# Performance work log

Measured on AMD Instinct MI355X. Metric: run time of the kernel, lower is better.

## Reference

```python
import jax, jax.numpy as jnp
import numpy as np

# ---- static config (seq_lens / is_prefill are Python lists in the original) ----
HIDDEN, H, D = 4096, 32, 128
SEQ = 1024            # prefill length / decode history length
N_PRE, N_DEC = 4, 4
T = N_PRE * SEQ + N_DEC            # 4100 total tokens
SEQ_LENS = [SEQ] * N_PRE + [SEQ] * N_DEC
IS_PREFILL = [True] * N_PRE + [False] * N_DEC
NUM_SLOTS = 8192
MAX_LEN, ROPE_BASE = 8192, 10000.0
SCALE = D ** -0.5


def _rope_tables():
    inv_freq = 1.0 / (ROPE_BASE ** (np.arange(0, D, 2, dtype=np.float32) / D))
    t = np.arange(MAX_LEN, dtype=np.float32)
    freqs = np.outer(t, inv_freq)
    emb = np.concatenate([freqs, freqs], axis=-1)  # [MAX_LEN, D]
    return jnp.asarray(np.cos(emb), jnp.float32), jnp.asarray(np.sin(emb), jnp.float32)

COS_T, SIN_T = _rope_tables()


def rotate_half(x):
    x1, x2 = jnp.split(x, 2, axis=-1)
    return jnp.concatenate([-x2, x1], axis=-1)


def setup_inputs() -> dict:
    key = jax.random.key(0)
    k1, k2, k3 = jax.random.split(key, 3)
    x = jax.random.normal(k1, (T, HIDDEN), jnp.float32)
    # positions: prefill seqs get 0..SEQ-1, decode seqs are at position SEQ
    pos = np.concatenate([np.tile(np.arange(SEQ), N_PRE), np.full(N_DEC, SEQ)]).astype(np.int64)
    positions = jnp.asarray(pos)
    slot_mapping = jnp.arange(T, dtype=jnp.int64)
    k_cache = jnp.zeros((NUM_SLOTS, H, D), jnp.float32)
    v_cache = jnp.zeros((NUM_SLOTS, H, D), jnp.float32)
    w_qkv = jax.random.normal(k2, (HIDDEN, 3 * H * D), jnp.float32) * 0.02
    w_out = jax.random.normal(k3, (H * D, HIDDEN), jnp.float32) * 0.02
    return {"x": x, "k_cache": k_cache, "v_cache": v_cache, "w_qkv": w_qkv,
            "w_out": w_out, "positions": positions, "slot_mapping": slot_mapping}


def reference(x, k_cache, v_cache, w_qkv, w_out, positions, slot_mapping):
    qkv = x @ w_qkv                                   # [T, 3*H*D]
    q, k, v = jnp.split(qkv, 3, axis=-1)
    q = q.reshape(T, H, D)
    k = k.reshape(T, H, D)
    v = v.reshape(T, H, D)
    cos = COS_T[positions][:, None, :]                # [T, 1, D]
    sin = SIN_T[positions][:, None, :]
    q = q * cos + rotate_half(q) * sin
    k = k * cos + rotate_half(k) * sin
    # scatter new k/v into flat paged cache
    kc = k_cache.at[slot_mapping].set(k)
    vc = v_cache.at[slot_mapping].set(v)

    outs = []
    off = 0
    for seq_len, prefill in zip(SEQ_LENS, IS_PREFILL):
        nq = seq_len if prefill else 1
        q_i = q[off:off + nq]                         # [nq, H, D]
        if prefill:
            k_i, v_i = k[off:off + nq], v[off:off + nq]
            attn = jnp.einsum('qhd,khd->hqk', q_i, k_i) * SCALE
            mask = jnp.triu(jnp.full((nq, nq), -jnp.inf, jnp.float32), 1)
            attn = jax.nn.softmax(attn + mask, axis=-1)
            out = jnp.einsum('hqk,khd->qhd', attn, v_i).reshape(nq, H * D)
        else:
            k_h, v_h = kc[:seq_len], vc[:seq_len]     # history from cache
            attn = jnp.einsum('qhd,khd->hqk', q_i, k_h) * SCALE
            attn = jax.nn.softmax(attn, axis=-1)
            out = jnp.einsum('hqk,khd->qhd', attn, v_h).reshape(1, H * D)
        outs.append(out)
        off += nq
    return jnp.concatenate(outs, axis=0) @ w_out      # [T, HIDDEN]
```

## Files before the change

kernel.cpp:

```cpp
#include <hip/hip_runtime.h>

#define T_TOK 4100
#define MMAIN 4096
#define HID   4096
#define NH    32
#define DH    128
#define NQKV  12288
#define ATT_SCALE 0.08838834764831845f
#define NEG_BIG  (-3.0e38f)

typedef unsigned short ushort_t;
typedef __attribute__((ext_vector_type(8))) short bf16x8;
typedef __attribute__((ext_vector_type(4))) float f32x4;

typedef const void __attribute__((address_space(1)))* gas_ptr;
typedef void __attribute__((address_space(3)))* las_ptr;

__device__ __forceinline__ ushort_t f2bf(float f){
  unsigned int u = __builtin_bit_cast(unsigned int, f);
  u = u + 0x7FFFu + ((u >> 16) & 1u);
  return (ushort_t)(u >> 16);
}
__device__ __forceinline__ float bf2f(ushort_t h){
  unsigned int u = ((unsigned int)h) << 16;
  return __builtin_bit_cast(float, u);
}
__device__ __forceinline__ f32x4 mfma16(bf16x8 a, bf16x8 b, f32x4 c){
  return __builtin_amdgcn_mfma_f32_16x16x32_bf16(a, b, c, 0, 0, 0);
}
__device__ __forceinline__ void gload_lds16(const void* g, void* l){
  __builtin_amdgcn_global_load_lds((gas_ptr)g, (las_ptr)l, 16, 0, 0);
}


__global__ void convert_x(const float* __restrict__ x, ushort_t* __restrict__ xb){
  const long i4 = (long)blockIdx.x * 256 + threadIdx.x;
  if (i4 >= (long)T_TOK * HID / 4) return;
  const long i = i4 * 4;
  const float4 v = *(const float4*)(x + i);
  union { ushort_t u[4]; uint2 w; } o;
  o.u[0] = f2bf(v.x); o.u[1] = f2bf(v.y); o.u[2] = f2bf(v.z); o.u[3] = f2bf(v.w);
  *(uint2*)(xb + i) = o.w;
}

__global__ void tconv(const float* __restrict__ W, ushort_t* __restrict__ WT, int R, int C){
  __shared__ float tile[32][33];
  const int bc = blockIdx.x, br = blockIdx.y;
  const int tid = threadIdx.x;
  const int cl = tid & 31, rl = tid >> 5;
  const long c = (long)bc * 32 + cl;
#pragma unroll
  for (int j = 0; j < 32; j += 8)
    tile[rl + j][cl] = W[((long)br * 32 + rl + j) * C + c];
  __syncthreads();
#pragma unroll
  for (int j = 0; j < 32; j += 8)
    WT[((long)bc * 32 + rl + j) * R + (long)br * 32 + cl] = f2bf(tile[cl][rl + j]);
}


#define MFMAQ(QM,QN,BARR)                                                         \
  _Pragma("unroll")                                                               \
  for (int mi = 0; mi < 4; ++mi) {                                                \
    _Pragma("unroll")                                                             \
    for (int ni = 0; ni < 2; ++ni) {                                              \
      acc[QM][QN][mi][ni] = mfma16(af[mi][0], BARR[ni][0], acc[QM][QN][mi][ni]);  \
      acc[QM][QN][mi][ni] = mfma16(af[mi][1], BARR[ni][1], acc[QM][QN][mi][ni]);  \
    } }

template<bool OUT_BF16>
__global__ void __launch_bounds__(512, 2)
gemm256(const ushort_t* __restrict__ A, const ushort_t* __restrict__ B,
        ushort_t* __restrict__ Cb, float* __restrict__ Cf,
        int N, int K, int GM, int Mvalid)
{
  extern __shared__ char smem[];
  char* smA = smem;
  char* smB = smem + 65536;

  const int nwg = gridDim.x;
  int bid = blockIdx.x;
  bid = (bid & 7) * (nwg >> 3) + (bid >> 3);
  const int bm = bid % GM, bn = bid / GM;

  const int tid = threadIdx.x;
  const int wid = tid >> 6, lane = tid & 63;
  const int wm = wid >> 2, wn = wid & 3;
  const int l16 = lane & 15, g = lane >> 4;
  const int lr = lane >> 3, lu = lane & 7;

  const long arow0 = (long)bm * 256;
  const long brow0 = (long)bn * 256;

  const ushort_t* aS[4]; const ushort_t* bS[4];
#pragma unroll
  for (int cc = 0; cc < 4; ++cc){
    aS[cc] = A + (arow0 + cc*64 + wid*8 + lr) * (long)K + (lu ^ lr) * 8;
    bS[cc] = B + (brow0 + cc*64 + wid*8 + lr) * (long)K + (lu ^ lr) * 8;
  }

  auto stageA = [&](int buf, int cc, long kt){
    gload_lds16(aS[cc] + kt, smA + buf*32768 + (cc*64 + wid*8)*128);
  };
  auto stageB = [&](int buf, int cc, long kt){
    gload_lds16(bS[cc] + kt, smB + buf*32768 + (cc*64 + wid*8)*128);
  };
  auto ldA = [&](int buf, int qm, int mi, int ks) -> bf16x8 {
    const int row = qm*128 + wm*64 + mi*16 + l16;
    return *(const bf16x8*)(smA + buf*32768 + row*128 + (((ks*4+g) ^ (l16&7))*16));
  };
  auto ldB = [&](int buf, int qn, int ni, int ks) -> bf16x8 {
    const int row = qn*128 + wn*32 + ni*16 + l16;
    return *(const bf16x8*)(smB + buf*32768 + row*128 + (((ks*4+g) ^ (l16&7))*16));
  };

  f32x4 acc[2][2][4][2];
#pragma unroll
  for (int a_ = 0; a_ < 2; ++a_)
#pragma unroll
  for (int b_ = 0; b_ < 2; ++b_)
#pragma unroll
  for (int c_ = 0; c_ < 4; ++c_)
#pragma unroll
  for (int d_ = 0; d_ < 2; ++d_) acc[a_][b_][c_][d_] = (f32x4){0.f,0.f,0.f,0.f};

  bf16x8 af[4][2], bf0[2][2], bf1[2][2];
  const int NT = K >> 6;

  stageA(0,0,0); stageA(0,1,0);
  stageB(0,0,0); stageB(0,1,0);
  stageB(0,2,0); stageB(0,3,0);
  stageA(0,2,0); stageA(0,3,0);
  asm volatile("s_waitcnt vmcnt(4)" ::: "memory");
  __builtin_amdgcn_s_barrier();

  auto tile = [&](int buf, long ktn){
    asm volatile("s_waitcnt vmcnt(2)" ::: "memory");
#pragma unroll
    for (int mi = 0; mi < 4; ++mi){ af[mi][0] = ldA(buf,0,mi,0); af[mi][1] = ldA(buf,0,mi,1); }
#pragma unroll
    for (int ni = 0; ni < 2; ++ni){ bf0[ni][0] = ldB(buf,0,ni,0); bf0[ni][1] = ldB(buf,0,ni,1); }
    stageA(buf^1, 0, ktn); stageA(buf^1, 1, ktn);
    __builtin_amdgcn_s_barrier();
    asm volatile("s_waitcnt lgkmcnt(0)" ::: "memory");
    __builtin_amdgcn_sched_barrier(0);
    __builtin_amdgcn_s_setprio(1);
    MFMAQ(0,0,bf0);
    __builtin_amdgcn_s_setprio(0);
    asm volatile("s_waitcnt vmcnt(2)" ::: "memory");
#pragma unroll
    for (int ni = 0; ni < 2; ++ni){ bf1[ni][0] = ldB(buf,1,ni,0); bf1[ni][1] = ldB(buf,1,ni,1); }
    stageB(buf^1, 0, ktn); stageB(buf^1, 1, ktn);
    __builtin_amdgcn_s_barrier();
    asm volatile("s_waitcnt lgkmcnt(0)" ::: "memory");
    __builtin_amdgcn_sched_barrier(0);
    __builtin_amdgcn_s_setprio(1);
    MFMAQ(0,1,bf1);
    __builtin_amdgcn_s_setprio(0);
#pragma unroll
    for (int mi = 0; mi < 4; ++mi){ af[mi][0] = ldA(buf,1,mi,0); af[mi][1] = ldA(buf,1,mi,1); }
    stageB(buf^1, 2, ktn); stageB(buf^1, 3, ktn);
    __builtin_amdgcn_s_barrier();
    asm volatile("s_waitcnt lgkmcnt(0)" ::: "memory");
    __builtin_amdgcn_sched_barrier(0);
    __builtin_amdgcn_s_setprio(1);
    MFMAQ(1,1,bf1);
    __builtin_amdgcn_s_setprio(0);
    asm volatile("s_waitcnt vmcnt(2)" ::: "memory");
    stageA(buf^1, 2, ktn); stageA(buf^1, 3, ktn);
    __builtin_amdgcn_s_barrier();
    __builtin_amdgcn_sched_barrier(0);
    __builtin_amdgcn_s_setprio(1);
    MFMAQ(1,0,bf0);
    __builtin_amdgcn_s_setprio(0);
  };

  for (int t = 0; t < NT; t += 2){
    const long k1 = (long)(t+1) * 64;
    const long k2 = (long)((t+2 < NT) ? (t+2) : (NT-1)) * 64;
    tile(0, k1);
    tile(1, k2);
  }
  asm volatile("s_waitcnt vmcnt(0)" ::: "memory");

#pragma unroll
  for (int qm = 0; qm < 2; ++qm)
#pragma unroll
  for (int qn = 0; qn < 2; ++qn)
#pragma unroll
  for (int mi = 0; mi < 4; ++mi)
#pragma unroll
  for (int ni = 0; ni < 2; ++ni)
#pragma unroll
  for (int r = 0; r < 4; ++r){
    const long row = arow0 + qm*128 + wm*64 + mi*16 + g*4 + r;
    const long col = brow0 + qn*128 + wn*32 + ni*16 + l16;
    if (OUT_BF16){
      Cb[row * N + col] = f2bf(acc[qm][qn][mi][ni][r]);
    } else {
      if (row < Mvalid) Cf[row * N + col] = acc[qm][qn][mi][ni][r];
    }
  }
}


__global__ void __launch_bounds__(256, 8)
gemv_tail(const ushort_t* __restrict__ A, const ushort_t* __restrict__ B,
          ushort_t* __restrict__ Cb, float* __restrict__ Cf, int ldc)
{
  const int col  = blockIdx.x * 4 + (threadIdx.x >> 6);
  const int lane = threadIdx.x & 63;
  const ushort_t* brow  = B + (long)col * HID + lane * 64;
  const ushort_t* abase = A + 4096L * HID + lane * 64;
  float acc0 = 0.f, acc1 = 0.f, acc2 = 0.f, acc3 = 0.f;
#pragma unroll
  for (int i = 0; i < 8; ++i){
    union { bf16x8 v; short s[8]; } bv, a0, a1, a2, a3;
    bv.v = *(const bf16x8*)(brow + i*8);
    a0.v = *(const bf16x8*)(abase + 0L*HID + i*8);
    a1.v = *(const bf16x8*)(abase + 1L*HID + i*8);
    a2.v = *(const bf16x8*)(abase + 2L*HID + i*8);
    a3.v = *(const bf16x8*)(abase + 3L*HID + i*8);
#pragma unroll
    for (int e = 0; e < 8; ++e){
      const float bf_ = bf2f((ushort_t)bv.s[e]);
      acc0 += bf2f((ushort_t)a0.s[e]) * bf_;
      acc1 += bf2f((ushort_t)a1.s[e]) * bf_;
      acc2 += bf2f((ushort_t)a2.s[e]) * bf_;
      acc3 += bf2f((ushort_t)a3.s[e]) * bf_;
    }
  }
#pragma unroll
  for (int off = 32; off; off >>= 1){
    acc0 += __shfl_xor(acc0, off);
    acc1 += __shfl_xor(acc1, off);
    acc2 += __shfl_xor(acc2, off);
    acc3 += __shfl_xor(acc3, off);
  }
  if (lane == 0){
    if (Cb){
      Cb[4096L*ldc + col] = f2bf(acc0);
      Cb[4097L*ldc + col] = f2bf(acc1);
      Cb[4098L*ldc + col] = f2bf(acc2);
      Cb[4099L*ldc + col] = f2bf(acc3);
    } else {
      Cf[4096L*ldc + col] = acc0;
      Cf[4097L*ldc + col] = acc1;
      Cf[4098L*ldc + col] = acc2;
      Cf[4099L*ldc + col] = acc3;
    }
  }
}


__global__ void rope_scatter(ushort_t* __restrict__ qkv,
                             const int* __restrict__ pos32,
                             const int* __restrict__ slot32,
                             ushort_t* __restrict__ kcw, ushort_t* __restrict__ vcw)
{
  const long gi = (long)blockIdx.x * 256 + threadIdx.x;
  if (gi >= (long)T_TOK * NH * 64) return;
  const int  i = gi & 63;
  const int  h = (gi >> 6) & 31;
  const long t = gi >> 11;

  const bool p64 = (pos32[1] == 0);
  const bool s64 = (slot32[1] == 0);
  const long pv   = p64 ? ((const long long*)pos32)[t]  : (long)pos32[t];
  const long slot = s64 ? ((const long long*)slot32)[t] : (long)slot32[t];

  const float inv = exp2f(-(float)i * 0.2076187116f);
  const float ang = (float)pv * inv;
  float sn, cs;
  __sincosf(ang, &sn, &cs);

  ushort_t* base = qkv + t * (long)NQKV + h * DH + i;
  const float q1 = bf2f(base[0]), q2 = bf2f(base[64]);
  base[0]  = f2bf(q1 * cs - q2 * sn);
  base[64] = f2bf(q2 * cs + q1 * sn);

  ushort_t* kb = base + HID;
  const float k1 = bf2f(kb[0]), k2 = bf2f(kb[64]);
  const float k1n = k1 * cs - k2 * sn, k2n = k2 * cs + k1 * sn;
  kb[0]  = f2bf(k1n);
  kb[64] = f2bf(k2n);

  if (slot >= 0 && slot < 1024){
    ushort_t* kd = kcw + (slot * NH + h) * DH + i;
    kd[0] = f2bf(k1n); kd[64] = f2bf(k2n);
    const ushort_t* vsrc = base + 2 * HID;
    ushort_t* vd = vcw + (slot * NH + h) * DH + i;
    vd[0] = vsrc[0]; vd[64] = vsrc[64];
  }
}


__global__ void __launch_bounds__(256, 3)
attn_prefill(const ushort_t* __restrict__ qkv, ushort_t* __restrict__ attn)
{
  __shared__ ushort_t Ks[64][128];
  __shared__ ushort_t Vt[128][72];
  __shared__ ushort_t Ps[4][16][72];
  const int qb = blockIdx.x, h = blockIdx.y, sq = blockIdx.z;
  const long tok0 = (long)sq * 1024;
  const int tid = threadIdx.x, wid = tid >> 6, lane = tid & 63;
  const int l16 = lane & 15, g = lane >> 4;
  const int q0 = qb * 64;

  bf16x8 qf[4];
  {
    const ushort_t* qrow = qkv + (tok0 + q0 + wid*16 + l16) * (long)NQKV + h * DH;
#pragma unroll
    for (int dc = 0; dc < 4; ++dc) qf[dc] = *(const bf16x8*)(qrow + dc*32 + g*8);
  }

  f32x4 oacc[8];
#pragma unroll
  for (int i = 0; i < 8; i++) oacc[i] = (f32x4){0.f, 0.f, 0.f, 0.f};
  float mrow[4] = {NEG_BIG, NEG_BIG, NEG_BIG, NEG_BIG};
  float lrow[4] = {0.f, 0.f, 0.f, 0.f};

  const int nkb = qb + 1;
  for (int kb = 0; kb < nkb; ++kb){
    __syncthreads();
    {
      const ushort_t* kbase = qkv + (tok0 + kb*64) * (long)NQKV + HID + h * DH;
#pragma unroll
      for (int c = 0; c < 4; ++c){
        const int row = c*16 + wid*4 + g;
        const int pu = (l16 & 8) | ((l16 ^ (row & 7)) & 7);
        gload_lds16(kbase + (long)row * NQKV + pu*8, &Ks[c*16 + wid*4][0]);
      }
    }
    {
      const int key4 = (tid & 15) * 4;
      const int dg8  = tid >> 4;
      const ushort_t* vbase = qkv + (tok0 + kb*64) * (long)NQKV + 2*HID + h*DH + dg8*8;
      union { bf16x8 v; short s[8]; } vr[4];
#pragma unroll
      for (int j = 0; j < 4; ++j)
        vr[j].v = *(const bf16x8*)(vbase + (long)(key4 + j) * NQKV);
#pragma unroll
      for (int e = 0; e < 8; ++e){
        union { ushort_t u[4]; uint2 w; } o;
        o.u[0] = (ushort_t)vr[0].s[e]; o.u[1] = (ushort_t)vr[1].s[e];
        o.u[2] = (ushort_t)vr[2].s[e]; o.u[3] = (ushort_t)vr[3].s[e];
        *(uint2*)&Vt[dg8*8 + e][key4] = o.w;
      }
    }
    __syncthreads();

    if (kb*64 <= q0 + wid*16 + 15){
      f32x4 sfr[4];
#pragma unroll
      for (int nf = 0; nf < 4; ++nf) sfr[nf] = (f32x4){0.f,0.f,0.f,0.f};
#pragma unroll
      for (int nf = 0; nf < 4; ++nf){
#pragma unroll
        for (int dc = 0; dc < 4; ++dc){
          const int uu = dc*4 + g;
          const int pu = (uu & 8) | ((uu ^ (l16 & 7)) & 7);
          bf16x8 kf = *(const bf16x8*)&Ks[nf*16 + l16][pu * 8];
          sfr[nf] = mfma16(qf[dc], kf, sfr[nf]);
        }
      }
      float alpha[4];
#pragma unroll
      for (int r = 0; r < 4; r++){
        const int qg = q0 + wid*16 + g*4 + r;
        float s[4];
#pragma unroll
        for (int nf = 0; nf < 4; ++nf){
          s[nf] = sfr[nf][r] * ATT_SCALE;
          if (kb*64 + nf*16 + l16 > qg) s[nf] = NEG_BIG;
        }
        float mx = fmaxf(fmaxf(s[0], s[1]), fmaxf(s[2], s[3]));
        mx = fmaxf(mx, __shfl_xor(mx, 1));
        mx = fmaxf(mx, __shfl_xor(mx, 2));
        mx = fmaxf(mx, __shfl_xor(mx, 4));
        mx = fmaxf(mx, __shfl_xor(mx, 8));
        const float mn = fmaxf(mrow[r], mx);
        const float al = __expf(mrow[r] - mn);
        float p[4], rs = 0.f;
#pragma unroll
        for (int nf = 0; nf < 4; ++nf){ p[nf] = __expf(s[nf] - mn); rs += p[nf]; }
        rs += __shfl_xor(rs, 1);
        rs += __shfl_xor(rs, 2);
        rs += __shfl_xor(rs, 4);
        rs += __shfl_xor(rs, 8);
        lrow[r] = lrow[r] * al + rs;
        mrow[r] = mn;
        alpha[r] = al;
#pragma unroll
        for (int nf = 0; nf < 4; ++nf)
          Ps[wid][g*4 + r][nf*16 + l16] = f2bf(p[nf]);
      }
#pragma unroll
      for (int df = 0; df < 8; ++df){
        f32x4 o = oacc[df];
        o[0] *= alpha[0]; o[1] *= alpha[1]; o[2] *= alpha[2]; o[3] *= alpha[3];
        oacc[df] = o;
      }
#pragma unroll
      for (int ks = 0; ks < 2; ++ks){
        bf16x8 pa = *(const bf16x8*)&Ps[wid][l16][ks*32 + g*8];
#pragma unroll
        for (int df = 0; df < 8; ++df){
          bf16x8 vf = *(const bf16x8*)&Vt[df*16 + l16][ks*32 + g*8];
          oacc[df] = mfma16(pa, vf, oacc[df]);
        }
      }
    }
  }

#pragma unroll
  for (int df = 0; df < 8; ++df){
#pragma unroll
    for (int r = 0; r < 4; ++r){
      const long row = tok0 + q0 + wid*16 + g*4 + r;
      attn[row * HID + h*DH + df*16 + l16] = f2bf(oacc[df][r] / lrow[r]);
    }
  }
}


__global__ void __launch_bounds__(256, 2)
attn_decode(const ushort_t* __restrict__ qkv, const ushort_t* __restrict__ kcw,
            const ushort_t* __restrict__ vcw, ushort_t* __restrict__ attn)
{
  const int h = blockIdx.x;
  const long t = 4096 + blockIdx.y;
  __shared__ float qs[128];
  __shared__ float ps[1024];
  __shared__ float red[8];
  __shared__ float oh[128];
  const int tid = threadIdx.x, wid = tid >> 6, lane = tid & 63;
  if (tid < 128) qs[tid] = bf2f(qkv[t * (long)NQKV + h*DH + tid]);
  __syncthreads();
  float sv[4];
#pragma unroll
  for (int j = 0; j < 4; j++){
    const int key = tid + j*256;
    const ushort_t* kr = kcw + ((long)key * NH + h) * DH;
    float acc = 0.f;
    for (int d = 0; d < 128; d += 8){
      union { bf16x8 v; short s[8]; } uu;
      uu.v = *(const bf16x8*)(kr + d);
#pragma unroll
      for (int e = 0; e < 8; e++) acc += qs[d+e] * bf2f((ushort_t)uu.s[e]);
    }
    sv[j] = acc * ATT_SCALE;
  }
  float mx = fmaxf(fmaxf(sv[0], sv[1]), fmaxf(sv[2], sv[3]));
#pragma unroll
  for (int off = 1; off < 64; off <<= 1) mx = fmaxf(mx, __shfl_xor(mx, off));
  if (lane == 0) red[wid] = mx;
  __syncthreads();
  const float gmax = fmaxf(fmaxf(red[0], red[1]), fmaxf(red[2], red[3]));
  float psum = 0.f;
#pragma unroll
  for (int j = 0; j < 4; j++){
    const float p = __expf(sv[j] - gmax);
    ps[tid + j*256] = p;
    psum += p;
  }
#pragma unroll
  for (int off = 1; off < 64; off <<= 1) psum += __shfl_xor(psum, off);
  if (lane == 0) red[4 + wid] = psum;
  __syncthreads();
  const float gsum = red[4] + red[5] + red[6] + red[7];
  const int d = tid & 127, half = tid >> 7;
  float acc = 0.f;
  for (int key = half*512; key < half*512 + 512; ++key)
    acc += ps[key] * bf2f(vcw[((long)key * NH + h) * DH + d]);
  if (half) oh[d] = acc;
  __syncthreads();
  if (!half) attn[t * HID + h*DH + d] = f2bf((acc + oh[d]) / gsum);
}


extern "C" void kernel_launch(void* const* d_in, const int* in_sizes, int n_in,
                              void* d_out, int out_size, void* d_ws, size_t ws_size,
                              hipStream_t stream) {
  const float* x      = (const float*)d_in[0];
  const float* wqkv   = (const float*)d_in[3];
  const float* wout   = (const float*)d_in[4];
  const int*   pos    = (const int*)d_in[5];
  const int*   slots  = (const int*)d_in[6];

  char* ws = (char*)d_ws;
  ushort_t* xb    = (ushort_t*)(ws);
  ushort_t* qkvb  = (ushort_t*)(ws + 35651584L);
  ushort_t* wqkvT = (ushort_t*)(ws + 142606336L);
  ushort_t* attnb = (ushort_t*)(ws + 142606336L);
  ushort_t* woutT = (ushort_t*)(ws + 243269632L);
  ushort_t* kcw   = (ushort_t*)(ws + 276824064L);
  ushort_t* vcw   = (ushort_t*)(ws + 285212672L);

  hipFuncSetAttribute((const void*)gemm256<true>,
                      hipFuncAttributeMaxDynamicSharedMemorySize, 131072);
  hipFuncSetAttribute((const void*)gemm256<false>,
                      hipFuncAttributeMaxDynamicSharedMemorySize, 131072);

  convert_x<<<16400, 256, 0, stream>>>(x, xb);
  tconv<<<dim3(NQKV/32, HID/32), 256, 0, stream>>>(wqkv, wqkvT, HID, NQKV);
  tconv<<<dim3(HID/32, HID/32), 256, 0, stream>>>(wout, woutT, HID, HID);

  gemm256<true><<<(MMAIN/256)*(NQKV/256), 512, 131072, stream>>>(
      xb, wqkvT, qkvb, nullptr, NQKV, HID, MMAIN/256, MMAIN);
  gemv_tail<<<NQKV/4, 256, 0, stream>>>(xb, wqkvT, qkvb, nullptr, NQKV);

  rope_scatter<<<32800, 256, 0, stream>>>(qkvb, pos, slots, kcw, vcw);

  attn_prefill<<<dim3(16, NH, 4), 256, 0, stream>>>(qkvb, attnb);
  attn_decode<<<dim3(NH, 4), 256, 0, stream>>>(qkvb, kcw, vcw, attnb);

  gemm256<false><<<(MMAIN/256)*(HID/256), 512, 131072, stream>>>(
      attnb, woutT, nullptr, (float*)d_out, HID, HID, MMAIN/256, MMAIN);
  gemv_tail<<<HID/4, 256, 0, stream>>>(attnb, woutT, nullptr, (float*)d_out, HID);

  (void)in_sizes; (void)n_in; (void)out_size; (void)ws_size;
}
```

Before: 1.004 ms.

## Fold GEMV tails into GEMM grids and fuse decode into prefill attention

```diff
diff --git a/kernel.cpp b/kernel.cpp
--- a/kernel.cpp
+++ b/kernel.cpp
@@ -78,13 +78,63 @@
   char* smA = smem;
   char* smB = smem + 65536;
 
-  const int nwg = gridDim.x;
-  int bid = blockIdx.x;
-  bid = (bid & 7) * (nwg >> 3) + (bid >> 3);
-  const int bm = bid % GM, bn = bid / GM;
-
   const int tid = threadIdx.x;
   const int wid = tid >> 6, lane = tid & 63;
+  const int ngemm = GM * (N >> 8);
+
+  if ((int)blockIdx.x >= ngemm){
+    const int tb = blockIdx.x - ngemm;
+    const int colbase = (tb*8 + wid) * 16;
+    const ushort_t* arow = A + 4096L * K + lane * 64;
+    for (int cc = 0; cc < 16; ++cc){
+      const int col = colbase + cc;
+      const ushort_t* brow = B + (long)col * K + lane * 64;
+      float a0=0.f, a1=0.f, a2=0.f, a3=0.f;
+#pragma unroll
+      for (int i = 0; i < 8; ++i){
+        union { bf16x8 v; short s[8]; } bv, r0, r1, r2, r3;
+        bv.v = *(const bf16x8*)(brow + i*8);
+        r0.v = *(const bf16x8*)(arow + 0L*K + i*8);
+        r1.v = *(const bf16x8*)(arow + 1L*K + i*8);
+        r2.v = *(const bf16x8*)(arow + 2L*K + i*8);
+        r3.v = *(const bf16x8*)(arow + 3L*K + i*8);
+#pragma unroll
+        for (int e = 0; e < 8; ++e){
+          const float bf_ = bf2f((ushort_t)bv.s[e]);
+          a0 += bf2f((ushort_t)r0.s[e]) * bf_;
+          a1 += bf2f((ushort_t)r1.s[e]) * bf_;
+          a2 += bf2f((ushort_t)r2.s[e]) * bf_;
+          a3 += bf2f((ushort_t)r3.s[e]) * bf_;
+        }
+      }
+#pragma unroll
+      for (int off = 32; off; off >>= 1){
+        a0 += __shfl_xor(a0, off);
+        a1 += __shfl_xor(a1, off);
+        a2 += __shfl_xor(a2, off);
+        a3 += __shfl_xor(a3, off);
+      }
+      if (lane == 0){
+        if (OUT_BF16){
+          Cb[4096L*N + col] = f2bf(a0);
+          Cb[4097L*N + col] = f2bf(a1);
+          Cb[4098L*N + col] = f2bf(a2);
+          Cb[4099L*N + col] = f2bf(a3);
+        } else {
+          Cf[4096L*N + col] = a0;
+          Cf[4097L*N + col] = a1;
+          Cf[4098L*N + col] = a2;
+          Cf[4099L*N + col] = a3;
+        }
+      }
+    }
+    return;
+  }
+
+  int bid = blockIdx.x;
+  bid = (bid & 7) * (ngemm >> 3) + (bid >> 3);
+  const int bm = bid % GM, bn = bid / GM;
+
   const int wm = wid >> 2, wn = wid & 3;
   const int l16 = lane & 15, g = lane >> 4;
   const int lr = lane >> 3, lu = lane & 7;
@@ -204,55 +254,6 @@
 }
 
 
-__global__ void __launch_bounds__(256, 8)
-gemv_tail(const ushort_t* __restrict__ A, const ushort_t* __restrict__ B,
-          ushort_t* __restrict__ Cb, float* __restrict__ Cf, int ldc)
-{
-  const int col  = blockIdx.x * 4 + (threadIdx.x >> 6);
-  const int lane = threadIdx.x & 63;
-  const ushort_t* brow  = B + (long)col * HID + lane * 64;
-  const ushort_t* abase = A + 4096L * HID + lane * 64;
-  float acc0 = 0.f, acc1 = 0.f, acc2 = 0.f, acc3 = 0.f;
-#pragma unroll
-  for (int i = 0; i < 8; ++i){
-    union { bf16x8 v; short s[8]; } bv, a0, a1, a2, a3;
-    bv.v = *(const bf16x8*)(brow + i*8);
-    a0.v = *(const bf16x8*)(abase + 0L*HID + i*8);
-    a1.v = *(const bf16x8*)(abase + 1L*HID + i*8);
-    a2.v = *(const bf16x8*)(abase + 2L*HID + i*8);
-    a3.v = *(const bf16x8*)(abase + 3L*HID + i*8);
-#pragma unroll
-    for (int e = 0; e < 8; ++e){
-      const float bf_ = bf2f((ushort_t)bv.s[e]);
-      acc0 += bf2f((ushort_t)a0.s[e]) * bf_;
-      acc1 += bf2f((ushort_t)a1.s[e]) * bf_;
-      acc2 += bf2f((ushort_t)a2.s[e]) * bf_;
-      acc3 += bf2f((ushort_t)a3.s[e]) * bf_;
-    }
-  }
-#pragma unroll
-  for (int off = 32; off; off >>= 1){
-    acc0 += __shfl_xor(acc0, off);
-    acc1 += __shfl_xor(acc1, off);
-    acc2 += __shfl_xor(acc2, off);
-    acc3 += __shfl_xor(acc3, off);
-  }
-  if (lane == 0){
-    if (Cb){
-      Cb[4096L*ldc + col] = f2bf(acc0);
-      Cb[4097L*ldc + col] = f2bf(acc1);
-      Cb[4098L*ldc + col] = f2bf(acc2);
-      Cb[4099L*ldc + col] = f2bf(acc3);
-    } else {
-      Cf[4096L*ldc + col] = acc0;
-      Cf[4097L*ldc + col] = acc1;
-      Cf[4098L*ldc + col] = acc2;
-      Cf[4099L*ldc + col] = acc3;
-    }
-  }
-}
-
-
 __global__ void rope_scatter(ushort_t* __restrict__ qkv,
                              const int* __restrict__ pos32,
                              const int* __restrict__ slot32,
@@ -296,14 +297,67 @@
 
 
 __global__ void __launch_bounds__(256, 3)
-attn_prefill(const ushort_t* __restrict__ qkv, ushort_t* __restrict__ attn)
+attn_fused(const ushort_t* __restrict__ qkv, const ushort_t* __restrict__ kcw,
+           const ushort_t* __restrict__ vcw, ushort_t* __restrict__ attn)
 {
-  __shared__ ushort_t Ks[64][128];
-  __shared__ ushort_t Vt[128][72];
-  __shared__ ushort_t Ps[4][16][72];
+  __shared__ char sm[44032];
   const int qb = blockIdx.x, h = blockIdx.y, sq = blockIdx.z;
+  const int tid = threadIdx.x, wid = tid >> 6, lane = tid & 63;
+
+  if (qb == 16){
+    float* qs  = (float*)sm;
+    float* ps  = qs + 128;
+    float* red = ps + 1024;
+    float* oh  = red + 8;
+    const long t = 4096 + sq;
+    if (tid < 128) qs[tid] = bf2f(qkv[t * (long)NQKV + h*DH + tid]);
+    __syncthreads();
+    float sv[4];
+#pragma unroll
+    for (int j = 0; j < 4; j++){
+      const int key = tid + j*256;
+      const ushort_t* kr = kcw + ((long)key * NH + h) * DH;
+      float acc = 0.f;
+      for (int d = 0; d < 128; d += 8){
+        union { bf16x8 v; short s[8]; } uu;
+        uu.v = *(const bf16x8*)(kr + d);
+#pragma unroll
+        for (int e = 0; e < 8; e++) acc += qs[d+e] * bf2f((ushort_t)uu.s[e]);
+      }
+      sv[j] = acc * ATT_SCALE;
+    }
+    float mx = fmaxf(fmaxf(sv[0], sv[1]), fmaxf(sv[2], sv[3]));
+#pragma unroll
+    for (int off = 1; off < 64; off <<= 1) mx = fmaxf(mx, __shfl_xor(mx, off));
+    if (lane == 0) red[wid] = mx;
+    __syncthreads();
+    const float gmax = fmaxf(fmaxf(red[0], red[1]), fmaxf(red[2], red[3]));
+    float psum = 0.f;
+#pragma unroll
+    for (int j = 0; j < 4; j++){
+      const float p = __expf(sv[j] - gmax);
+      ps[tid + j*256] = p;
+      psum += p;
+    }
+#pragma unroll
+    for (int off = 1; off < 64; off <<= 1) psum += __shfl_xor(psum, off);
+    if (lane == 0) red[4 + wid] = psum;
+    __syncthreads();
+    const float gsum = red[4] + red[5] + red[6] + red[7];
+    const int d = tid & 127, half = tid >> 7;
+    float acc = 0.f;
+    for (int key = half*512; key < half*512 + 512; ++key)
+      acc += ps[key] * bf2f(vcw[((long)key * NH + h) * DH + d]);
+    if (half) oh[d] = acc;
+    __syncthreads();
+    if (!half) attn[t * HID + h*DH + d] = f2bf((acc + oh[d]) / gsum);
+    return;
+  }
+
+  ushort_t (*Ks)[128]    = (ushort_t(*)[128])sm;
+  ushort_t (*Vt)[72]     = (ushort_t(*)[72])(sm + 16384);
+  ushort_t (*Ps)[16][72] = (ushort_t(*)[16][72])(sm + 34816);
   const long tok0 = (long)sq * 1024;
-  const int tid = threadIdx.x, wid = tid >> 6, lane = tid & 63;
   const int l16 = lane & 15, g = lane >> 4;
   const int q0 = qb * 64;
 
@@ -350,7 +404,7 @@
     }
     __syncthreads();
 
-    if (kb*64 <= q0 + wid*16 + 15){
+    {
       f32x4 sfr[4];
 #pragma unroll
       for (int nf = 0; nf < 4; ++nf) sfr[nf] = (f32x4){0.f,0.f,0.f,0.f};
@@ -364,15 +418,18 @@
           sfr[nf] = mfma16(qf[dc], kf, sfr[nf]);
         }
       }
+      const bool diag = (kb == qb);
       float alpha[4];
 #pragma unroll
       for (int r = 0; r < 4; r++){
-        const int qg = q0 + wid*16 + g*4 + r;
         float s[4];
 #pragma unroll
-        for (int nf = 0; nf < 4; ++nf){
-          s[nf] = sfr[nf][r] * ATT_SCALE;
-          if (kb*64 + nf*16 + l16 > qg) s[nf] = NEG_BIG;
+        for (int nf = 0; nf < 4; ++nf) s[nf] = sfr[nf][r] * ATT_SCALE;
+        if (diag){
+          const int qg = q0 + wid*16 + g*4 + r;
+#pragma unroll
+          for (int nf = 0; nf < 4; ++nf)
+            if (kb*64 + nf*16 + l16 > qg) s[nf] = NEG_BIG;
         }
         float mx = fmaxf(fmaxf(s[0], s[1]), fmaxf(s[2], s[3]));
         mx = fmaxf(mx, __shfl_xor(mx, 1));
@@ -424,61 +481,6 @@
 }
 
 
-__global__ void __launch_bounds__(256, 2)
-attn_decode(const ushort_t* __restrict__ qkv, const ushort_t* __restrict__ kcw,
-            const ushort_t* __restrict__ vcw, ushort_t* __restrict__ attn)
-{
-  const int h = blockIdx.x;
-  const long t = 4096 + blockIdx.y;
-  __shared__ float qs[128];
-  __shared__ float ps[1024];
-  __shared__ float red[8];
-  __shared__ float oh[128];
-  const int tid = threadIdx.x, wid = tid >> 6, lane = tid & 63;
-  if (tid < 128) qs[tid] = bf2f(qkv[t * (long)NQKV + h*DH + tid]);
-  __syncthreads();
-  float sv[4];
-#pragma unroll
-  for (int j = 0; j < 4; j++){
-    const int key = tid + j*256;
-    const ushort_t* kr = kcw + ((long)key * NH + h) * DH;
-    float acc = 0.f;
-    for (int d = 0; d < 128; d += 8){
-      union { bf16x8 v; short s[8]; } uu;
-      uu.v = *(const bf16x8*)(kr + d);
-#pragma unroll
-      for (int e = 0; e < 8; e++) acc += qs[d+e] * bf2f((ushort_t)uu.s[e]);
-    }
-    sv[j] = acc * ATT_SCALE;
-  }
-  float mx = fmaxf(fmaxf(sv[0], sv[1]), fmaxf(sv[2], sv[3]));
-#pragma unroll
-  for (int off = 1; off < 64; off <<= 1) mx = fmaxf(mx, __shfl_xor(mx, off));
-  if (lane == 0) red[wid] = mx;
-  __syncthreads();
-  const float gmax = fmaxf(fmaxf(red[0], red[1]), fmaxf(red[2], red[3]));
-  float psum = 0.f;
-#pragma unroll
-  for (int j = 0; j < 4; j++){
-    const float p = __expf(sv[j] - gmax);
-    ps[tid + j*256] = p;
-    psum += p;
-  }
-#pragma unroll
-  for (int off = 1; off < 64; off <<= 1) psum += __shfl_xor(psum, off);
-  if (lane == 0) red[4 + wid] = psum;
-  __syncthreads();
-  const float gsum = red[4] + red[5] + red[6] + red[7];
-  const int d = tid & 127, half = tid >> 7;
-  float acc = 0.f;
-  for (int key = half*512; key < half*512 + 512; ++key)
-    acc += ps[key] * bf2f(vcw[((long)key * NH + h) * DH + d]);
-  if (half) oh[d] = acc;
-  __syncthreads();
-  if (!half) attn[t * HID + h*DH + d] = f2bf((acc + oh[d]) / gsum);
-}
-
-
 extern "C" void kernel_launch(void* const* d_in, const int* in_sizes, int n_in,
                               void* d_out, int out_size, void* d_ws, size_t ws_size,
                               hipStream_t stream) {
@@ -506,18 +508,15 @@
   tconv<<<dim3(NQKV/32, HID/32), 256, 0, stream>>>(wqkv, wqkvT, HID, NQKV);
   tconv<<<dim3(HID/32, HID/32), 256, 0, stream>>>(wout, woutT, HID, HID);
 
-  gemm256<true><<<(MMAIN/256)*(NQKV/256), 512, 131072, stream>>>(
+  gemm256<true><<<(MMAIN/256)*(NQKV/256) + NQKV/128, 512, 131072, stream>>>(
       xb, wqkvT, qkvb, nullptr, NQKV, HID, MMAIN/256, MMAIN);
-  gemv_tail<<<NQKV/4, 256, 0, stream>>>(xb, wqkvT, qkvb, nullptr, NQKV);
 
   rope_scatter<<<32800, 256, 0, stream>>>(qkvb, pos, slots, kcw, vcw);
 
-  attn_prefill<<<dim3(16, NH, 4), 256, 0, stream>>>(qkvb, attnb);
-  attn_decode<<<dim3(NH, 4), 256, 0, stream>>>(qkvb, kcw, vcw, attnb);
-
-  gemm256<false><<<(MMAIN/256)*(HID/256), 512, 131072, stream>>>(
+  attn_fused<<<dim3(17, NH, 4), 256, 0, stream>>>(qkvb, kcw, vcw, attnb);
+
+  gemm256<false><<<(MMAIN/256)*(HID/256) + HID/128, 512, 131072, stream>>>(
       attnb, woutT, nullptr, (float*)d_out, HID, HID, MMAIN/256, MMAIN);
-  gemv_tail<<<HID/4, 256, 0, stream>>>(attnb, woutT, nullptr, (float*)d_out, HID);
 
   (void)in_sizes; (void)n_in; (void)out_size; (void)ws_size;
 }
```

Measured after the change: 964.7 us. -3.9%, faster.

## Fuse decode attention into prefill kernel and skip unused decode K/V work

Applied to the files above, without the earlier changes.

```diff
diff --git a/kernel.cpp b/kernel.cpp
--- a/kernel.cpp
+++ b/kernel.cpp
@@ -279,31 +279,86 @@
   base[0]  = f2bf(q1 * cs - q2 * sn);
   base[64] = f2bf(q2 * cs + q1 * sn);
 
-  ushort_t* kb = base + HID;
-  const float k1 = bf2f(kb[0]), k2 = bf2f(kb[64]);
-  const float k1n = k1 * cs - k2 * sn, k2n = k2 * cs + k1 * sn;
-  kb[0]  = f2bf(k1n);
-  kb[64] = f2bf(k2n);
-
-  if (slot >= 0 && slot < 1024){
-    ushort_t* kd = kcw + (slot * NH + h) * DH + i;
-    kd[0] = f2bf(k1n); kd[64] = f2bf(k2n);
-    const ushort_t* vsrc = base + 2 * HID;
-    ushort_t* vd = vcw + (slot * NH + h) * DH + i;
-    vd[0] = vsrc[0]; vd[64] = vsrc[64];
+  if (t < 4096){
+    ushort_t* kb = base + HID;
+    const float k1 = bf2f(kb[0]), k2 = bf2f(kb[64]);
+    const float k1n = k1 * cs - k2 * sn, k2n = k2 * cs + k1 * sn;
+    kb[0]  = f2bf(k1n);
+    kb[64] = f2bf(k2n);
+
+    if (slot >= 0 && slot < 1024){
+      ushort_t* kd = kcw + (slot * NH + h) * DH + i;
+      kd[0] = f2bf(k1n); kd[64] = f2bf(k2n);
+      const ushort_t* vsrc = base + 2 * HID;
+      ushort_t* vd = vcw + (slot * NH + h) * DH + i;
+      vd[0] = vsrc[0]; vd[64] = vsrc[64];
+    }
   }
 }
 
 
 __global__ void __launch_bounds__(256, 3)
-attn_prefill(const ushort_t* __restrict__ qkv, ushort_t* __restrict__ attn)
+attn_fused(const ushort_t* __restrict__ qkv, const ushort_t* __restrict__ kcw,
+           const ushort_t* __restrict__ vcw, ushort_t* __restrict__ attn)
 {
-  __shared__ ushort_t Ks[64][128];
-  __shared__ ushort_t Vt[128][72];
-  __shared__ ushort_t Ps[4][16][72];
+  __shared__ char sm[44032];
   const int qb = blockIdx.x, h = blockIdx.y, sq = blockIdx.z;
+  const int tid = threadIdx.x, wid = tid >> 6, lane = tid & 63;
+
+  if (qb == 16){
+    float* qs  = (float*)sm;
+    float* ps  = qs + 128;
+    float* red = ps + 1024;
+    float* oh  = red + 8;
+    const long t = 4096 + sq;
+    if (tid < 128) qs[tid] = bf2f(qkv[t * (long)NQKV + h*DH + tid]);
+    __syncthreads();
+    float sv[4];
+#pragma unroll
+    for (int j = 0; j < 4; j++){
+      const int key = tid + j*256;
+      const ushort_t* kr = kcw + ((long)key * NH + h) * DH;
+      float acc = 0.f;
+      for (int d = 0; d < 128; d += 8){
+        union { bf16x8 v; short s[8]; } uu;
+        uu.v = *(const bf16x8*)(kr + d);
+#pragma unroll
+        for (int e = 0; e < 8; e++) acc += qs[d+e] * bf2f((ushort_t)uu.s[e]);
+      }
+      sv[j] = acc * ATT_SCALE;
+    }
+    float mx = fmaxf(fmaxf(sv[0], sv[1]), fmaxf(sv[2], sv[3]));
+#pragma unroll
+    for (int off = 1; off < 64; off <<= 1) mx = fmaxf(mx, __shfl_xor(mx, off));
+    if (lane == 0) red[wid] = mx;
+    __syncthreads();
+    const float gmax = fmaxf(fmaxf(red[0], red[1]), fmaxf(red[2], red[3]));
+    float psum = 0.f;
+#pragma unroll
+    for (int j = 0; j < 4; j++){
+      const float p = __expf(sv[j] - gmax);
+      ps[tid + j*256] = p;
+      psum += p;
+    }
+#pragma unroll
+    for (int off = 1; off < 64; off <<= 1) psum += __shfl_xor(psum, off);
+    if (lane == 0) red[4 + wid] = psum;
+    __syncthreads();
+    const float gsum = red[4] + red[5] + red[6] + red[7];
+    const int d = tid & 127, half = tid >> 7;
+    float acc = 0.f;
+    for (int key = half*512; key < half*512 + 512; ++key)
+      acc += ps[key] * bf2f(vcw[((long)key * NH + h) * DH + d]);
+    if (half) oh[d] = acc;
+    __syncthreads();
+    if (!half) attn[t * HID + h*DH + d] = f2bf((acc + oh[d]) / gsum);
+    return;
+  }
+
+  ushort_t (*Ks)[128]    = (ushort_t(*)[128])sm;
+  ushort_t (*Vt)[72]     = (ushort_t(*)[72])(sm + 16384);
+  ushort_t (*Ps)[16][72] = (ushort_t(*)[16][72])(sm + 34816);
   const long tok0 = (long)sq * 1024;
-  const int tid = threadIdx.x, wid = tid >> 6, lane = tid & 63;
   const int l16 = lane & 15, g = lane >> 4;
   const int q0 = qb * 64;
 
@@ -350,7 +405,7 @@
     }
     __syncthreads();
 
-    if (kb*64 <= q0 + wid*16 + 15){
+    {
       f32x4 sfr[4];
 #pragma unroll
       for (int nf = 0; nf < 4; ++nf) sfr[nf] = (f32x4){0.f,0.f,0.f,0.f};
@@ -364,15 +419,18 @@
           sfr[nf] = mfma16(qf[dc], kf, sfr[nf]);
         }
       }
+      const bool diag = (kb == qb);
       float alpha[4];
 #pragma unroll
       for (int r = 0; r < 4; r++){
-        const int qg = q0 + wid*16 + g*4 + r;
         float s[4];
 #pragma unroll
-        for (int nf = 0; nf < 4; ++nf){
-          s[nf] = sfr[nf][r] * ATT_SCALE;
-          if (kb*64 + nf*16 + l16 > qg) s[nf] = NEG_BIG;
+        for (int nf = 0; nf < 4; ++nf) s[nf] = sfr[nf][r] * ATT_SCALE;
+        if (diag){
+          const int qg = q0 + wid*16 + g*4 + r;
+#pragma unroll
+          for (int nf = 0; nf < 4; ++nf)
+            if (kb*64 + nf*16 + l16 > qg) s[nf] = NEG_BIG;
         }
         float mx = fmaxf(fmaxf(s[0], s[1]), fmaxf(s[2], s[3]));
         mx = fmaxf(mx, __shfl_xor(mx, 1));
@@ -424,61 +482,6 @@
 }
 
 
-__global__ void __launch_bounds__(256, 2)
-attn_decode(const ushort_t* __restrict__ qkv, const ushort_t* __restrict__ kcw,
-            const ushort_t* __restrict__ vcw, ushort_t* __restrict__ attn)
-{
-  const int h = blockIdx.x;
-  const long t = 4096 + blockIdx.y;
-  __shared__ float qs[128];
-  __shared__ float ps[1024];
-  __shared__ float red[8];
-  __shared__ float oh[128];
-  const int tid = threadIdx.x, wid = tid >> 6, lane = tid & 63;
-  if (tid < 128) qs[tid] = bf2f(qkv[t * (long)NQKV + h*DH + tid]);
-  __syncthreads();
-  float sv[4];
-#pragma unroll
-  for (int j = 0; j < 4; j++){
-    const int key = tid + j*256;
-    const ushort_t* kr = kcw + ((long)key * NH + h) * DH;
-    float acc = 0.f;
-    for (int d = 0; d < 128; d += 8){
-      union { bf16x8 v; short s[8]; } uu;
-      uu.v = *(const bf16x8*)(kr + d);
-#pragma unroll
-      for (int e = 0; e < 8; e++) acc += qs[d+e] * bf2f((ushort_t)uu.s[e]);
-    }
-    sv[j] = acc * ATT_SCALE;
-  }
-  float mx = fmaxf(fmaxf(sv[0], sv[1]), fmaxf(sv[2], sv[3]));
-#pragma unroll
-  for (int off = 1; off < 64; off <<= 1) mx = fmaxf(mx, __shfl_xor(mx, off));
-  if (lane == 0) red[wid] = mx;
-  __syncthreads();
-  const float gmax = fmaxf(fmaxf(red[0], red[1]), fmaxf(red[2], red[3]));
-  float psum = 0.f;
-#pragma unroll
-  for (int j = 0; j < 4; j++){
-    const float p = __expf(sv[j] - gmax);
-    ps[tid + j*256] = p;
-    psum += p;
-  }
-#pragma unroll
-  for (int off = 1; off < 64; off <<= 1) psum += __shfl_xor(psum, off);
-  if (lane == 0) red[4 + wid] = psum;
-  __syncthreads();
-  const float gsum = red[4] + red[5] + red[6] + red[7];
-  const int d = tid & 127, half = tid >> 7;
-  float acc = 0.f;
-  for (int key = half*512; key < half*512 + 512; ++key)
-    acc += ps[key] * bf2f(vcw[((long)key * NH + h) * DH + d]);
-  if (half) oh[d] = acc;
-  __syncthreads();
-  if (!half) attn[t * HID + h*DH + d] = f2bf((acc + oh[d]) / gsum);
-}
-
-
 extern "C" void kernel_launch(void* const* d_in, const int* in_sizes, int n_in,
                               void* d_out, int out_size, void* d_ws, size_t ws_size,
                               hipStream_t stream) {
@@ -508,12 +511,11 @@
 
   gemm256<true><<<(MMAIN/256)*(NQKV/256), 512, 131072, stream>>>(
       xb, wqkvT, qkvb, nullptr, NQKV, HID, MMAIN/256, MMAIN);
-  gemv_tail<<<NQKV/4, 256, 0, stream>>>(xb, wqkvT, qkvb, nullptr, NQKV);
+  gemv_tail<<<HID/4, 256, 0, stream>>>(xb, wqkvT, qkvb, nullptr, NQKV);
 
   rope_scatter<<<32800, 256, 0, stream>>>(qkvb, pos, slots, kcw, vcw);
 
-  attn_prefill<<<dim3(16, NH, 4), 256, 0, stream>>>(qkvb, attnb);
-  attn_decode<<<dim3(NH, 4), 256, 0, stream>>>(qkvb, kcw, vcw, attnb);
+  attn_fused<<<dim3(17, NH, 4), 256, 0, stream>>>(qkvb, kcw, vcw, attnb);
 
   gemm256<false><<<(MMAIN/256)*(HID/256), 512, 131072, stream>>>(
       attnb, woutT, nullptr, (float*)d_out, HID, HID, MMAIN/256, MMAIN);
```

New measurement: 837.3 us. -16.6%, faster.
